# Kernel tuning notes

Hardware: AMD Instinct MI355X
Metric: run time of the kernel (lower is better)

The kernel has to match this reference:

```python
import jax, jax.numpy as jnp
import numpy as np
from jax import lax

INPUT_SIZE = 64          # classifier ROI size (init kwarg)
IMG = 640                # source image H=W
PROV, ALPHA, AD = 38, 25, 35
CONF_THRES, IOU_THRES = 0.25, 0.45
MAX_DET = 300            # yolov5 NMS max detections
FLAT = 16 * (INPUT_SIZE // 2) ** 2  # 16384


def setup_inputs() -> dict:
    key = jax.random.key(0)
    ks = jax.random.split(key, 12)
    B, N = 1, 25200
    xy = jax.random.uniform(ks[0], (B, N, 2), minval=32.0, maxval=608.0)
    wh = jax.random.uniform(ks[1], (B, N, 2), minval=16.0, maxval=128.0)
    obj = jax.random.uniform(ks[2], (B, N, 1))
    cls = jax.random.uniform(ks[3], (B, N, 1))
    preds = jnp.concatenate([xy, wh, obj, cls], axis=-1)  # [1,N,6] xywh+obj+cls
    image = jax.random.normal(ks[4], (B, 3, IMG, IMG), dtype=jnp.float32)
    W_conv = 0.1 * jax.random.normal(ks[5], (16, 3, 3, 3), dtype=jnp.float32)
    b_conv = jnp.zeros((16,), jnp.float32)
    W1 = 0.01 * jax.random.normal(ks[6], (8, FLAT, 128), dtype=jnp.float32)
    b1 = jnp.zeros((8, 128), jnp.float32)
    W2p = 0.05 * jax.random.normal(ks[7], (128, PROV), dtype=jnp.float32)
    b2p = jnp.zeros((PROV,), jnp.float32)
    W2a = 0.05 * jax.random.normal(ks[8], (128, ALPHA), dtype=jnp.float32)
    b2a = jnp.zeros((ALPHA,), jnp.float32)
    W2d = 0.05 * jax.random.normal(ks[9], (6, 128, AD), dtype=jnp.float32)
    b2d = jnp.zeros((6, AD), jnp.float32)
    return {"preds": preds, "image": image, "W_conv": W_conv, "b_conv": b_conv,
            "W1": W1, "b1": b1, "W2p": W2p, "b2p": b2p, "W2a": W2a, "b2a": b2a,
            "W2d": W2d, "b2d": b2d}


def _pairwise_iou(b):
    # b: [K,4] xyxy
    x1, y1, x2, y2 = b[:, 0], b[:, 1], b[:, 2], b[:, 3]
    area = (x2 - x1) * (y2 - y1)
    iw = jnp.clip(jnp.minimum(x2[:, None], x2[None, :]) - jnp.maximum(x1[:, None], x1[None, :]), 0.0)
    ih = jnp.clip(jnp.minimum(y2[:, None], y2[None, :]) - jnp.maximum(y1[:, None], y1[None, :]), 0.0)
    inter = iw * ih
    return inter / (area[:, None] + area[None, :] - inter + 1e-7)


def reference(preds, image, W_conv, b_conv, W1, b1, W2p, b2p, W2a, b2a, W2d, b2d):
    # ---- NMS (yolov5-style, single class) ----
    p = preds[0]                                   # [N,6]
    score = p[:, 4] * p[:, 5]                      # obj_conf * cls_conf
    xy, wh = p[:, 0:2], p[:, 2:4]
    boxes = jnp.concatenate([xy - wh / 2, xy + wh / 2], axis=-1)  # xyxy
    masked = jnp.where(score > CONF_THRES, score, -jnp.inf)
    top_s, idx = lax.top_k(masked, MAX_DET)        # sorted desc
    b = boxes[idx]                                 # [K,4]
    valid = top_s > CONF_THRES
    ious = _pairwise_iou(b)                        # [K,K]
    ar = jnp.arange(MAX_DET)

    def body(i, keep):
        sup = jnp.any((ious[i] > IOU_THRES) & keep & (ar < i))
        return keep.at[i].set(keep[i] & jnp.logical_not(sup))

    keep = lax.fori_loop(0, MAX_DET, body, valid)  # greedy suppression

    # ---- fixed-size ROI crop at box top-left (clipped) ----
    x1 = jnp.clip(jnp.round(b[:, 0]).astype(jnp.int32), 0, IMG - INPUT_SIZE)
    y1 = jnp.clip(jnp.round(b[:, 1]).astype(jnp.int32), 0, IMG - INPUT_SIZE)
    img0 = image[0]                                # [3,H,W]
    crops = jax.vmap(lambda y, x: lax.dynamic_slice(img0, (0, y, x), (3, INPUT_SIZE, INPUT_SIZE)))(y1, x1)

    # ---- LicensePlateClassifier: conv->relu->maxpool->flatten->8 heads ----
    conv = lax.conv_general_dilated(crops, W_conv, (1, 1), 'SAME',
                                    dimension_numbers=('NCHW', 'OIHW', 'NCHW'))
    conv = jax.nn.relu(conv + b_conv[None, :, None, None])
    pooled = lax.reduce_window(conv, -jnp.inf, lax.max, (1, 1, 2, 2), (1, 1, 2, 2), 'VALID')
    feats = pooled.reshape(MAX_DET, FLAT)          # NCHW flatten == torch.flatten(x,1)
    h = jax.nn.relu(jnp.einsum('kf,hfd->hkd', feats, W1) + b1[:, None, :])  # [8,K,128]
    out_p = h[0] @ W2p + b2p                       # [K,38]
    out_a = h[1] @ W2a + b2a                       # [K,25]
    out_d = jnp.einsum('hkd,hdo->hko', h[2:], W2d) + b2d[:, None, :]        # [6,K,35]
    out_d = out_d.transpose(1, 0, 2).reshape(MAX_DET, 6 * AD)
    logits = jnp.concatenate([out_p, out_a, out_d], axis=1)  # [K,273]
    return logits * keep.astype(logits.dtype)[:, None]
```

## Files before the change

kernel.cpp:

```cpp
#include <hip/hip_runtime.h>

#define N_PRED 25200
#define CONF 0.25f
#define IOU_THR 0.45f
#define MAXD 300
#define IMGW 640
#define CROPW 64
#define HISTN 16640
#define KSPLIT 16

typedef float f32x4 __attribute__((ext_vector_type(4)));
typedef short s16x8 __attribute__((ext_vector_type(8)));
typedef unsigned long long u64;

#define OFF_HIST   0u
#define OFF_CNT    66560u
#define OFF_CUT    66624u
#define OFF_CAND   66816u
#define CTRL_BYTES 75008u
#define OFF_BOXES  75008u
#define OFF_XY1    79872u
#define OFF_VALID  82432u
#define OFF_KEEP   83712u
#define OFF_SUP    84992u
#define OFF_H      97024u
#define OFF_FEATS  1325824u
#define OFF_PART   11811584u

__device__ inline unsigned short f2bf(float x) {
  unsigned u = __float_as_uint(x);
  u += 0x7FFFu + ((u >> 16) & 1u);
  return (unsigned short)(u >> 16);
}

__global__ __launch_bounds__(256) void k_hist(const float* __restrict__ preds,
                                              unsigned* __restrict__ hist) {
  int i = blockIdx.x * 256 + threadIdx.x;
  if (i >= N_PRED) return;
  float s = preds[i * 6 + 4] * preds[i * 6 + 5];
  if (s > CONF) atomicAdd(&hist[__float_as_uint(s) >> 16], 1u);
}

__global__ __launch_bounds__(256) void k_findcut(const unsigned* __restrict__ hist,
                                                 unsigned* __restrict__ cut) {
  __shared__ unsigned s[256];
  int t = threadIdx.x;
  int base = t * 65;
  unsigned local = 0;
  for (int i = 0; i < 65; ++i) local += hist[base + i];
  s[t] = local;
  __syncthreads();
  for (int off = 1; off < 256; off <<= 1) {
    unsigned add = (t + off < 256) ? s[t + off] : 0u;
    __syncthreads();
    s[t] += add;
    __syncthreads();
  }
  unsigned incl = s[t];
  unsigned excl = (t < 255) ? s[t + 1] : 0u;
  if (incl >= (unsigned)MAXD && excl < (unsigned)MAXD) {
    unsigned acc = excl, res = 0u;
    #pragma unroll
    for (int ii = 64; ii >= 0; --ii) {
      acc += hist[base + ii];
      if (res == 0u && acc >= (unsigned)MAXD) res = (unsigned)(base + ii);
    }
    cut[0] = res;
  }
}

__global__ __launch_bounds__(256) void k_compact(const float* __restrict__ preds,
                                                 const unsigned* __restrict__ cut,
                                                 unsigned* __restrict__ cnt,
                                                 u64* __restrict__ cand) {
  int i = blockIdx.x * 256 + threadIdx.x;
  if (i >= N_PRED) return;
  float s = preds[i * 6 + 4] * preds[i * 6 + 5];
  if (s <= CONF) return;
  unsigned bits = __float_as_uint(s);
  if ((bits >> 16) < cut[0]) return;
  unsigned pos = atomicAdd(cnt, 1u);
  if (pos < 1024u)
    cand[pos] = ((u64)bits << 32) | (u64)(0xFFFFFFFFu - (unsigned)i);
}

__global__ __launch_bounds__(1024) void k_sortprep(const float* __restrict__ preds,
                                                   const u64* __restrict__ cand,
                                                   float* __restrict__ boxes,
                                                   int* __restrict__ xy1,
                                                   float* __restrict__ validf) {
  __shared__ u64 sk[1024];
  int t = threadIdx.x;
  sk[t] = cand[t];
  __syncthreads();
  for (int k = 2; k <= 1024; k <<= 1)
    for (int j = k >> 1; j > 0; j >>= 1) {
      int p = t ^ j;
      if (p > t) {
        u64 a = sk[t], b = sk[p];
        bool up = ((t & k) == 0);
        bool sw = up ? (a < b) : (a > b);
        if (sw) { sk[t] = b; sk[p] = a; }
      }
      __syncthreads();
    }
  if (t < MAXD) {
    u64 key = sk[t];
    if (key != 0ull) {
      int idx = (int)(0xFFFFFFFFu - (unsigned)(key & 0xFFFFFFFFull));
      float cx = preds[idx * 6 + 0], cy = preds[idx * 6 + 1];
      float w  = preds[idx * 6 + 2], h  = preds[idx * 6 + 3];
      float x1 = cx - w * 0.5f, y1 = cy - h * 0.5f;
      float x2 = cx + w * 0.5f, y2 = cy + h * 0.5f;
      boxes[t * 4 + 0] = x1; boxes[t * 4 + 1] = y1;
      boxes[t * 4 + 2] = x2; boxes[t * 4 + 3] = y2;
      int xi = (int)rintf(x1); xi = min(max(xi, 0), IMGW - CROPW);
      int yi = (int)rintf(y1); yi = min(max(yi, 0), IMGW - CROPW);
      xy1[t * 2 + 0] = xi; xy1[t * 2 + 1] = yi;
      validf[t] = 1.0f;
    } else {
      boxes[t * 4 + 0] = 0.f; boxes[t * 4 + 1] = 0.f;
      boxes[t * 4 + 2] = 0.f; boxes[t * 4 + 3] = 0.f;
      xy1[t * 2 + 0] = 0; xy1[t * 2 + 1] = 0;
      validf[t] = 0.f;
    }
  }
}

__global__ __launch_bounds__(320) void k_iou(const float* __restrict__ boxes,
                                             u64* __restrict__ sup) {
  int i = blockIdx.x, t = threadIdx.x;
  int w = t >> 6, lane = t & 63;
  f32x4 bi = *(const f32x4*)&boxes[i * 4];
  f32x4 bj = (t < MAXD) ? *(const f32x4*)&boxes[t * 4]
                        : (f32x4){0.f, 0.f, 0.f, 0.f};
  float ar  = (bi[2] - bi[0]) * (bi[3] - bi[1]);
  float arj = (bj[2] - bj[0]) * (bj[3] - bj[1]);
  float iw = fmaxf(fminf(bi[2], bj[2]) - fmaxf(bi[0], bj[0]), 0.f);
  float ih = fmaxf(fminf(bi[3], bj[3]) - fmaxf(bi[1], bj[1]), 0.f);
  float inter = iw * ih;
  float iou = inter / (ar + arj - inter + 1e-7f);
  u64 bm = __ballot((t < MAXD) && (iou > IOU_THR));
  if (lane == 0) sup[i * 5 + w] = bm;
}

__global__ __launch_bounds__(64) void k_nms(const u64* __restrict__ sup,
                                            const float* __restrict__ validf,
                                            float* __restrict__ keepf) {
  int lane = threadIdx.x;
  u64 srow[5][5];
  #pragma unroll
  for (int c = 0; c < 5; ++c)
    #pragma unroll
    for (int ww = 0; ww < 5; ++ww) srow[c][ww] = 0ull;
  #pragma unroll
  for (int c = 0; c < 5; ++c) {
    int i = c * 64 + lane;
    if (i < MAXD) {
      #pragma unroll
      for (int ww = 0; ww <= c; ++ww) srow[c][ww] = sup[i * 5 + ww];
    }
  }
  u64 validm[5];
  #pragma unroll
  for (int c = 0; c < 5; ++c) {
    int i = c * 64 + lane;
    float vf = (i < MAXD) ? validf[i] : 0.f;
    validm[c] = __ballot(vf > 0.5f);
  }
  u64 kw0 = 0, kw1 = 0, kw2 = 0, kw3 = 0;
  #pragma unroll
  for (int c = 0; c < 5; ++c) {
    bool ext = ((srow[c][0] & kw0) | (srow[c][1] & kw1) |
                (srow[c][2] & kw2) | (srow[c][3] & kw3)) != 0ull;
    u64 alive = validm[c] & __ballot(!ext);
    unsigned mlo = (unsigned)srow[c][c], mhi = (unsigned)(srow[c][c] >> 32);
    u64 rem = alive;
    while (rem) {
      int b = (int)__builtin_ctzll(rem);
      u64 gt = (b == 63) ? 0ull : (~0ull << (b + 1));
      u64 mi = ((u64)(unsigned)__builtin_amdgcn_readlane((int)mhi, b) << 32) |
               (u64)(unsigned)__builtin_amdgcn_readlane((int)mlo, b);
      alive &= ~(mi & gt);
      rem = alive & gt;
    }
    int i = c * 64 + lane;
    if (i < MAXD) keepf[i] = ((alive >> lane) & 1ull) ? 1.f : 0.f;
    if (c == 0) kw0 = alive;
    else if (c == 1) kw1 = alive;
    else if (c == 2) kw2 = alive;
    else if (c == 3) kw3 = alive;
  }
}

__global__ __launch_bounds__(256) void k_cropconv(const float* __restrict__ image,
                                                  const float* __restrict__ Wc,
                                                  const float* __restrict__ bc,
                                                  const int* __restrict__ xy1,
                                                  short* __restrict__ feats) {
  __shared__ __align__(16) float crop[3][10][68];
  int det = blockIdx.x, sl = blockIdx.y, tid = threadIdx.x;
  int pr0 = sl * 4;
  int gyBase = pr0 * 2 - 1;
  int ch = tid >> 4, px = tid & 15;

  float w[27];
  #pragma unroll
  for (int i = 0; i < 27; i++) w[i] = Wc[ch * 27 + i];
  float bias = bc[ch];

  int x0 = xy1[det * 2 + 0], y0 = xy1[det * 2 + 1];
  float sv[8];
  #pragma unroll
  for (int i = 0; i < 8; i++) {
    int u = tid + i * 256;
    float v = 0.f;
    if (u < 1920) {
      int row = u >> 6, x = u & 63;
      int c = row / 10, ry = row - c * 10;
      int gy = gyBase + ry;
      if (gy >= 0 && gy < CROPW)
        v = image[(size_t)c * (IMGW * IMGW) + (y0 + gy) * IMGW + x0 + x];
    }
    sv[i] = v;
  }
  if (tid < 120) {
    int row = tid >> 2, e = tid & 3;
    int c = row / 10, ry = row - c * 10;
    crop[c][ry][(e == 0) ? 0 : (64 + e)] = 0.f;
  }
  #pragma unroll
  for (int i = 0; i < 8; i++) {
    int u = tid + i * 256;
    if (u < 1920) {
      int row = u >> 6, x = u & 63;
      int c = row / 10, ry = row - c * 10;
      crop[c][ry][x + 1] = sv[i];
    }
  }
  __syncthreads();
  #pragma unroll
  for (int pr = 0; pr < 4; pr++) {
    float acc0[4] = {0.f, 0.f, 0.f, 0.f};
    float acc1[4] = {0.f, 0.f, 0.f, 0.f};
    #pragma unroll
    for (int c = 0; c < 3; c++) {
      #pragma unroll
      for (int r = 0; r < 4; r++) {
        const float* rp = &crop[c][2 * pr + r][4 * px];
        f32x4 v4 = *(const f32x4*)rp;
        float2 v2 = *(const float2*)(rp + 4);
        float in[6] = {v4[0], v4[1], v4[2], v4[3], v2.x, v2.y};
        if (r <= 2) {
          const float w0 = w[c * 9 + r * 3], w1 = w[c * 9 + r * 3 + 1],
                      w2 = w[c * 9 + r * 3 + 2];
          #pragma unroll
          for (int q = 0; q < 4; q++)
            acc0[q] += in[q] * w0 + in[q + 1] * w1 + in[q + 2] * w2;
        }
        if (r >= 1) {
          const float w0 = w[c * 9 + (r - 1) * 3], w1 = w[c * 9 + (r - 1) * 3 + 1],
                      w2 = w[c * 9 + (r - 1) * 3 + 2];
          #pragma unroll
          for (int q = 0; q < 4; q++)
            acc1[q] += in[q] * w0 + in[q + 1] * w1 + in[q + 2] * w2;
        }
      }
    }
    float m0 = fmaxf(fmaxf(acc0[0], acc0[1]), fmaxf(acc1[0], acc1[1]));
    float m1 = fmaxf(fmaxf(acc0[2], acc0[3]), fmaxf(acc1[2], acc1[3]));
    unsigned lo = f2bf(fmaxf(m0 + bias, 0.f));
    unsigned hi = f2bf(fmaxf(m1 + bias, 0.f));
    *(unsigned*)&feats[(size_t)det * 16384 + ch * 1024 + (pr0 + pr) * 32 + 2 * px] =
        lo | (hi << 16);
  }
}

__global__ __launch_bounds__(512, 2) void k_gemm(const short* __restrict__ feats,
                                                 const float* __restrict__ W1,
                                                 float* __restrict__ part) {
  __shared__ __align__(16) short As[2][320 * 64];
  int tid = threadIdx.x;
  int wid = tid >> 6, lane = tid & 63;
  int wm = wid & 3, wn = wid >> 2;
  int lr = lane & 15, kg = lane >> 4;
  int ks = blockIdx.x, hd = blockIdx.y, dh = blockIdx.z;
  const int f0 = ks * 1024, d0 = dh * 64;
  const float* w1h = W1 + (size_t)hd * 16384 * 128;

  f32x4 acc[5][2];
  #pragma unroll
  for (int i = 0; i < 5; i++)
    #pragma unroll
    for (int j = 0; j < 2; j++) acc[i][j] = (f32x4){0.f, 0.f, 0.f, 0.f};

  s16x8 aR[5];
  #pragma unroll
  for (int i = 0; i < 5; i++) {
    int ch = tid + i * 512, m = ch >> 3, c = ch & 7;
    aR[i] = *(const s16x8*)(feats + (size_t)m * 16384 + f0 + c * 8);
  }
  const float* bp = w1h + (size_t)(f0 + kg * 8) * 128 + d0 + wn * 32 + lr;
  float bF[2][2][8];
  #pragma unroll
  for (int k32 = 0; k32 < 2; k32++)
    #pragma unroll
    for (int nf = 0; nf < 2; nf++)
      #pragma unroll
      for (int j = 0; j < 8; j++)
        bF[k32][nf][j] = bp[(k32 * 32 + j) * 128 + nf * 16];
  #pragma unroll
  for (int i = 0; i < 5; i++) {
    int ch = tid + i * 512, m = ch >> 3, c = ch & 7;
    *(s16x8*)((char*)&As[0][0] + m * 128 + ((c ^ (m & 7)) << 4)) = aR[i];
  }
  __syncthreads();

  for (int t = 0; t < 16; ++t) {
    int cur = t & 1;
    s16x8 bfr[2][2];
    #pragma unroll
    for (int k32 = 0; k32 < 2; k32++)
      #pragma unroll
      for (int nf = 0; nf < 2; nf++)
        #pragma unroll
        for (int j = 0; j < 8; j++)
          bfr[k32][nf][j] = (short)f2bf(bF[k32][nf][j]);
    bool pf = (t + 1) < 16;
    if (pf) {
      int f1 = f0 + (t + 1) * 64;
      #pragma unroll
      for (int i = 0; i < 5; i++) {
        int ch = tid + i * 512, m = ch >> 3, c = ch & 7;
        aR[i] = *(const s16x8*)(feats + (size_t)m * 16384 + f1 + c * 8);
      }
      const float* bp2 = bp + (size_t)(t + 1) * 64 * 128;
      #pragma unroll
      for (int k32 = 0; k32 < 2; k32++)
        #pragma unroll
        for (int nf = 0; nf < 2; nf++)
          #pragma unroll
          for (int j = 0; j < 8; j++)
            bF[k32][nf][j] = bp2[(k32 * 32 + j) * 128 + nf * 16];
    }
    #pragma unroll
    for (int k32 = 0; k32 < 2; ++k32) {
      s16x8 af[5];
      #pragma unroll
      for (int mf = 0; mf < 5; ++mf) {
        int row = wm * 80 + mf * 16 + lr;
        int c = k32 * 4 + kg;
        af[mf] = *(const s16x8*)((const char*)&As[cur][0] + row * 128 + ((c ^ (row & 7)) << 4));
      }
      #pragma unroll
      for (int nf = 0; nf < 2; ++nf)
        #pragma unroll
        for (int mf = 0; mf < 5; ++mf)
          acc[mf][nf] = __builtin_amdgcn_mfma_f32_16x16x32_bf16(af[mf], bfr[k32][nf], acc[mf][nf], 0, 0, 0);
    }
    if (pf) {
      #pragma unroll
      for (int i = 0; i < 5; i++) {
        int ch = tid + i * 512, m = ch >> 3, c = ch & 7;
        *(s16x8*)((char*)&As[cur ^ 1][0] + m * 128 + ((c ^ (m & 7)) << 4)) = aR[i];
      }
      __syncthreads();
    }
  }
  #pragma unroll
  for (int mf = 0; mf < 5; ++mf)
    #pragma unroll
    for (int nf = 0; nf < 2; ++nf)
      #pragma unroll
      for (int r = 0; r < 4; ++r) {
        int m = wm * 80 + mf * 16 + kg * 4 + r;
        int d = d0 + wn * 32 + nf * 16 + lr;
        part[(((size_t)ks * 8 + hd) * 320 + m) * 128 + d] = acc[mf][nf][r];
      }
}

__global__ __launch_bounds__(256) void k_reduce(const float* __restrict__ part,
                                                const float* __restrict__ b1,
                                                float* __restrict__ h) {
  int o4 = blockIdx.x * 256 + threadIdx.x;
  int d4 = o4 & 31;
  int k = (o4 >> 5) % 300;
  int hh = o4 / (32 * 300);
  f32x4 s = (f32x4){0.f, 0.f, 0.f, 0.f};
  #pragma unroll
  for (int ksp = 0; ksp < KSPLIT; ksp++) {
    f32x4 v = *(const f32x4*)&part[(((size_t)ksp * 8 + hh) * 320 + k) * 128 + d4 * 4];
    s[0] += v[0]; s[1] += v[1]; s[2] += v[2]; s[3] += v[3];
  }
  f32x4 b = *(const f32x4*)&b1[hh * 128 + d4 * 4];
  f32x4 r;
  #pragma unroll
  for (int j = 0; j < 4; j++) r[j] = fmaxf(s[j] + b[j], 0.f);
  *(f32x4*)&h[((size_t)hh * 300 + k) * 128 + d4 * 4] = r;
}

__global__ __launch_bounds__(320) void k_fc2(const float* __restrict__ h,
                                             const float* __restrict__ keepf,
                                             const float* __restrict__ W2p,
                                             const float* __restrict__ b2p,
                                             const float* __restrict__ W2a,
                                             const float* __restrict__ b2a,
                                             const float* __restrict__ W2d,
                                             const float* __restrict__ b2d,
                                             float* __restrict__ out) {
  int det = blockIdx.x, t = threadIdx.x;
  __shared__ float hl[1024];
  for (int i = t; i < 1024; i += 320) {
    int hh = i >> 7, d = i & 127;
    hl[i] = h[((size_t)hh * 300 + det) * 128 + d];
  }
  __syncthreads();
  if (t >= 273) return;
  float kf = keepf[det];
  float s = 0.f, bias;
  if (t < 38) {
    const float* hp = hl;
    for (int d = 0; d < 128; d++) s += hp[d] * W2p[d * 38 + t];
    bias = b2p[t];
  } else if (t < 63) {
    int c = t - 38;
    const float* hp = hl + 128;
    for (int d = 0; d < 128; d++) s += hp[d] * W2a[d * 25 + c];
    bias = b2a[c];
  } else {
    int u = t - 63, j = u / 35, o = u - j * 35;
    const float* hp = hl + (2 + j) * 128;
    for (int d = 0; d < 128; d++) s += hp[d] * W2d[((size_t)j * 128 + d) * 35 + o];
    bias = b2d[j * 35 + o];
  }
  out[det * 273 + t] = (s + bias) * kf;
}

extern "C" void kernel_launch(void* const* d_in, const int* in_sizes, int n_in,
                              void* d_out, int out_size, void* d_ws, size_t ws_size,
                              hipStream_t stream) {
  (void)in_sizes; (void)n_in; (void)out_size; (void)ws_size;
  const float* preds = (const float*)d_in[0];
  const float* image = (const float*)d_in[1];
  const float* Wc    = (const float*)d_in[2];
  const float* bc    = (const float*)d_in[3];
  const float* W1    = (const float*)d_in[4];
  const float* b1    = (const float*)d_in[5];
  const float* W2p   = (const float*)d_in[6];
  const float* b2p   = (const float*)d_in[7];
  const float* W2a   = (const float*)d_in[8];
  const float* b2a   = (const float*)d_in[9];
  const float* W2d   = (const float*)d_in[10];
  const float* b2d   = (const float*)d_in[11];

  char* ws = (char*)d_ws;
  unsigned* hist   = (unsigned*)(ws + OFF_HIST);
  unsigned* cnt    = (unsigned*)(ws + OFF_CNT);
  unsigned* cut    = (unsigned*)(ws + OFF_CUT);
  u64*      cand   = (u64*)(ws + OFF_CAND);
  float*    boxes  = (float*)(ws + OFF_BOXES);
  int*      xy1    = (int*)(ws + OFF_XY1);
  float*    validf = (float*)(ws + OFF_VALID);
  float*    keepf  = (float*)(ws + OFF_KEEP);
  u64*      sup    = (u64*)(ws + OFF_SUP);
  float*    hbuf   = (float*)(ws + OFF_H);
  short*    feats  = (short*)(ws + OFF_FEATS);
  float*    part   = (float*)(ws + OFF_PART);
  float*    out    = (float*)d_out;

  hipMemsetAsync(ws, 0, CTRL_BYTES, stream);
  k_hist<<<(N_PRED + 255) / 256, 256, 0, stream>>>(preds, hist);
  k_findcut<<<1, 256, 0, stream>>>(hist, cut);
  k_compact<<<(N_PRED + 255) / 256, 256, 0, stream>>>(preds, cut, cnt, cand);
  k_sortprep<<<1, 1024, 0, stream>>>(preds, cand, boxes, xy1, validf);
  k_iou<<<MAXD, 320, 0, stream>>>(boxes, sup);
  k_nms<<<1, 64, 0, stream>>>(sup, validf, keepf);
  k_cropconv<<<dim3(300, 8), 256, 0, stream>>>(image, Wc, bc, xy1, feats);
  k_gemm<<<dim3(KSPLIT, 8, 2), 512, 0, stream>>>(feats, W1, part);
  k_reduce<<<300, 256, 0, stream>>>(part, b1, hbuf);
  k_fc2<<<MAXD, 320, 0, stream>>>(hbuf, keepf, W2p, b2p, W2a, b2a, W2d, b2d, out);
}
```

Baseline: 123.9 us.

## Fuse NMS pipeline kernels into one cooperative kernel with grid syncs

Replaces six separate NMS-stage launches (histogram, cut search, compaction, sort, IoU, greedy NMS) with a single cooperative kernel of 32 blocks of 1024 threads that uses grid.sync between phases. The goal is to remove per-launch overhead and inter-kernel gaps on this latency-bound chain. The cost is that grid-wide barriers may be slower than kernel boundaries, fewer blocks run the IoU stage, and the cut search now scans 17 bins per thread across 1024 threads.

```diff
diff --git a/kernel.cpp b/kernel.cpp
--- a/kernel.cpp
+++ b/kernel.cpp
@@ -1,4 +1,7 @@
 #include <hip/hip_runtime.h>
+#include <hip/hip_cooperative_groups.h>
+
+namespace cg = cooperative_groups;
 
 #define N_PRED 25200
 #define CONF 0.25f
@@ -8,6 +11,7 @@
 #define CROPW 64
 #define HISTN 16640
 #define KSPLIT 16
+#define DET_BLOCKS 32
 
 typedef float f32x4 __attribute__((ext_vector_type(4)));
 typedef short s16x8 __attribute__((ext_vector_type(8)));
@@ -33,163 +37,182 @@
   return (unsigned short)(u >> 16);
 }
 
-__global__ __launch_bounds__(256) void k_hist(const float* __restrict__ preds,
-                                              unsigned* __restrict__ hist) {
-  int i = blockIdx.x * 256 + threadIdx.x;
-  if (i >= N_PRED) return;
-  float s = preds[i * 6 + 4] * preds[i * 6 + 5];
-  if (s > CONF) atomicAdd(&hist[__float_as_uint(s) >> 16], 1u);
-}
-
-__global__ __launch_bounds__(256) void k_findcut(const unsigned* __restrict__ hist,
-                                                 unsigned* __restrict__ cut) {
-  __shared__ unsigned s[256];
-  int t = threadIdx.x;
-  int base = t * 65;
-  unsigned local = 0;
-  for (int i = 0; i < 65; ++i) local += hist[base + i];
-  s[t] = local;
+__global__ __launch_bounds__(1024) void k_detect(const float* __restrict__ preds,
+                                                 unsigned* __restrict__ hist,
+                                                 unsigned* __restrict__ cut,
+                                                 unsigned* __restrict__ cnt,
+                                                 u64* __restrict__ cand,
+                                                 float* __restrict__ boxes,
+                                                 int* __restrict__ xy1,
+                                                 float* __restrict__ validf,
+                                                 u64* __restrict__ sup,
+                                                 float* __restrict__ keepf) {
+  cg::grid_group grid = cg::this_grid();
+  __shared__ unsigned su[1024];
+  __shared__ u64 sk[1024];
+  __shared__ __align__(16) float sbf[MAXD * 4];
+  int tid = threadIdx.x, bid = blockIdx.x;
+  int gt = bid * 1024 + tid;
+
+  if (gt < N_PRED) {
+    float s = preds[gt * 6 + 4] * preds[gt * 6 + 5];
+    if (s > CONF) atomicAdd(&hist[__float_as_uint(s) >> 16], 1u);
+  }
+  __threadfence();
+  grid.sync();
+
+  if (bid == 0) {
+    int base = tid * 17;
+    unsigned local = 0;
+    for (int i = 0; i < 17; ++i) {
+      int idx = base + i;
+      if (idx < HISTN) local += hist[idx];
+    }
+    su[tid] = local;
+    __syncthreads();
+    for (int off = 1; off < 1024; off <<= 1) {
+      unsigned add = (tid + off < 1024) ? su[tid + off] : 0u;
+      __syncthreads();
+      su[tid] += add;
+      __syncthreads();
+    }
+    unsigned incl = su[tid];
+    unsigned excl = (tid < 1023) ? su[tid + 1] : 0u;
+    if (incl >= (unsigned)MAXD && excl < (unsigned)MAXD) {
+      unsigned acc = excl, res = 0u;
+      for (int ii = 16; ii >= 0; --ii) {
+        int idx = base + ii;
+        if (idx < HISTN) {
+          acc += hist[idx];
+          if (res == 0u && acc >= (unsigned)MAXD) res = (unsigned)idx;
+        }
+      }
+      cut[0] = res;
+    }
+  }
+  __threadfence();
+  grid.sync();
+
+  unsigned cutv = cut[0];
+  if (gt < N_PRED) {
+    float s = preds[gt * 6 + 4] * preds[gt * 6 + 5];
+    if (s > CONF) {
+      unsigned bits = __float_as_uint(s);
+      if ((bits >> 16) >= cutv) {
+        unsigned pos = atomicAdd(cnt, 1u);
+        if (pos < 1024u)
+          cand[pos] = ((u64)bits << 32) | (u64)(0xFFFFFFFFu - (unsigned)gt);
+      }
+    }
+  }
+  __threadfence();
+  grid.sync();
+
+  if (bid == 0) {
+    sk[tid] = cand[tid];
+    __syncthreads();
+    for (int k = 2; k <= 1024; k <<= 1)
+      for (int j = k >> 1; j > 0; j >>= 1) {
+        int p = tid ^ j;
+        if (p > tid) {
+          u64 a = sk[tid], b = sk[p];
+          bool up = ((tid & k) == 0);
+          bool sw = up ? (a < b) : (a > b);
+          if (sw) { sk[tid] = b; sk[p] = a; }
+        }
+        __syncthreads();
+      }
+    if (tid < MAXD) {
+      u64 key = sk[tid];
+      if (key != 0ull) {
+        int idx = (int)(0xFFFFFFFFu - (unsigned)(key & 0xFFFFFFFFull));
+        float cx = preds[idx * 6 + 0], cy = preds[idx * 6 + 1];
+        float w  = preds[idx * 6 + 2], h  = preds[idx * 6 + 3];
+        float x1 = cx - w * 0.5f, y1 = cy - h * 0.5f;
+        float x2 = cx + w * 0.5f, y2 = cy + h * 0.5f;
+        boxes[tid * 4 + 0] = x1; boxes[tid * 4 + 1] = y1;
+        boxes[tid * 4 + 2] = x2; boxes[tid * 4 + 3] = y2;
+        int xi = (int)rintf(x1); xi = min(max(xi, 0), IMGW - CROPW);
+        int yi = (int)rintf(y1); yi = min(max(yi, 0), IMGW - CROPW);
+        xy1[tid * 2 + 0] = xi; xy1[tid * 2 + 1] = yi;
+        validf[tid] = 1.0f;
+      } else {
+        boxes[tid * 4 + 0] = 0.f; boxes[tid * 4 + 1] = 0.f;
+        boxes[tid * 4 + 2] = 0.f; boxes[tid * 4 + 3] = 0.f;
+        xy1[tid * 2 + 0] = 0; xy1[tid * 2 + 1] = 0;
+        validf[tid] = 0.f;
+      }
+    }
+  }
+  __threadfence();
+  grid.sync();
+
+  for (int i = tid; i < MAXD * 4; i += 1024) sbf[i] = boxes[i];
   __syncthreads();
-  for (int off = 1; off < 256; off <<= 1) {
-    unsigned add = (t + off < 256) ? s[t + off] : 0u;
-    __syncthreads();
-    s[t] += add;
-    __syncthreads();
-  }
-  unsigned incl = s[t];
-  unsigned excl = (t < 255) ? s[t + 1] : 0u;
-  if (incl >= (unsigned)MAXD && excl < (unsigned)MAXD) {
-    unsigned acc = excl, res = 0u;
-    #pragma unroll
-    for (int ii = 64; ii >= 0; --ii) {
-      acc += hist[base + ii];
-      if (res == 0u && acc >= (unsigned)MAXD) res = (unsigned)(base + ii);
-    }
-    cut[0] = res;
-  }
-}
-
-__global__ __launch_bounds__(256) void k_compact(const float* __restrict__ preds,
-                                                 const unsigned* __restrict__ cut,
-                                                 unsigned* __restrict__ cnt,
-                                                 u64* __restrict__ cand) {
-  int i = blockIdx.x * 256 + threadIdx.x;
-  if (i >= N_PRED) return;
-  float s = preds[i * 6 + 4] * preds[i * 6 + 5];
-  if (s <= CONF) return;
-  unsigned bits = __float_as_uint(s);
-  if ((bits >> 16) < cut[0]) return;
-  unsigned pos = atomicAdd(cnt, 1u);
-  if (pos < 1024u)
-    cand[pos] = ((u64)bits << 32) | (u64)(0xFFFFFFFFu - (unsigned)i);
-}
-
-__global__ __launch_bounds__(1024) void k_sortprep(const float* __restrict__ preds,
-                                                   const u64* __restrict__ cand,
-                                                   float* __restrict__ boxes,
-                                                   int* __restrict__ xy1,
-                                                   float* __restrict__ validf) {
-  __shared__ u64 sk[1024];
-  int t = threadIdx.x;
-  sk[t] = cand[t];
-  __syncthreads();
-  for (int k = 2; k <= 1024; k <<= 1)
-    for (int j = k >> 1; j > 0; j >>= 1) {
-      int p = t ^ j;
-      if (p > t) {
-        u64 a = sk[t], b = sk[p];
-        bool up = ((t & k) == 0);
-        bool sw = up ? (a < b) : (a > b);
-        if (sw) { sk[t] = b; sk[p] = a; }
-      }
-      __syncthreads();
-    }
-  if (t < MAXD) {
-    u64 key = sk[t];
-    if (key != 0ull) {
-      int idx = (int)(0xFFFFFFFFu - (unsigned)(key & 0xFFFFFFFFull));
-      float cx = preds[idx * 6 + 0], cy = preds[idx * 6 + 1];
-      float w  = preds[idx * 6 + 2], h  = preds[idx * 6 + 3];
-      float x1 = cx - w * 0.5f, y1 = cy - h * 0.5f;
-      float x2 = cx + w * 0.5f, y2 = cy + h * 0.5f;
-      boxes[t * 4 + 0] = x1; boxes[t * 4 + 1] = y1;
-      boxes[t * 4 + 2] = x2; boxes[t * 4 + 3] = y2;
-      int xi = (int)rintf(x1); xi = min(max(xi, 0), IMGW - CROPW);
-      int yi = (int)rintf(y1); yi = min(max(yi, 0), IMGW - CROPW);
-      xy1[t * 2 + 0] = xi; xy1[t * 2 + 1] = yi;
-      validf[t] = 1.0f;
-    } else {
-      boxes[t * 4 + 0] = 0.f; boxes[t * 4 + 1] = 0.f;
-      boxes[t * 4 + 2] = 0.f; boxes[t * 4 + 3] = 0.f;
-      xy1[t * 2 + 0] = 0; xy1[t * 2 + 1] = 0;
-      validf[t] = 0.f;
-    }
-  }
-}
-
-__global__ __launch_bounds__(320) void k_iou(const float* __restrict__ boxes,
-                                             u64* __restrict__ sup) {
-  int i = blockIdx.x, t = threadIdx.x;
-  int w = t >> 6, lane = t & 63;
-  f32x4 bi = *(const f32x4*)&boxes[i * 4];
-  f32x4 bj = (t < MAXD) ? *(const f32x4*)&boxes[t * 4]
-                        : (f32x4){0.f, 0.f, 0.f, 0.f};
-  float ar  = (bi[2] - bi[0]) * (bi[3] - bi[1]);
-  float arj = (bj[2] - bj[0]) * (bj[3] - bj[1]);
-  float iw = fmaxf(fminf(bi[2], bj[2]) - fmaxf(bi[0], bj[0]), 0.f);
-  float ih = fmaxf(fminf(bi[3], bj[3]) - fmaxf(bi[1], bj[1]), 0.f);
-  float inter = iw * ih;
-  float iou = inter / (ar + arj - inter + 1e-7f);
-  u64 bm = __ballot((t < MAXD) && (iou > IOU_THR));
-  if (lane == 0) sup[i * 5 + w] = bm;
-}
-
-__global__ __launch_bounds__(64) void k_nms(const u64* __restrict__ sup,
-                                            const float* __restrict__ validf,
-                                            float* __restrict__ keepf) {
-  int lane = threadIdx.x;
-  u64 srow[5][5];
-  #pragma unroll
-  for (int c = 0; c < 5; ++c)
-    #pragma unroll
-    for (int ww = 0; ww < 5; ++ww) srow[c][ww] = 0ull;
-  #pragma unroll
-  for (int c = 0; c < 5; ++c) {
-    int i = c * 64 + lane;
-    if (i < MAXD) {
-      #pragma unroll
-      for (int ww = 0; ww <= c; ++ww) srow[c][ww] = sup[i * 5 + ww];
-    }
-  }
-  u64 validm[5];
-  #pragma unroll
-  for (int c = 0; c < 5; ++c) {
-    int i = c * 64 + lane;
-    float vf = (i < MAXD) ? validf[i] : 0.f;
-    validm[c] = __ballot(vf > 0.5f);
-  }
-  u64 kw0 = 0, kw1 = 0, kw2 = 0, kw3 = 0;
-  #pragma unroll
-  for (int c = 0; c < 5; ++c) {
-    bool ext = ((srow[c][0] & kw0) | (srow[c][1] & kw1) |
-                (srow[c][2] & kw2) | (srow[c][3] & kw3)) != 0ull;
-    u64 alive = validm[c] & __ballot(!ext);
-    unsigned mlo = (unsigned)srow[c][c], mhi = (unsigned)(srow[c][c] >> 32);
-    u64 rem = alive;
-    while (rem) {
-      int b = (int)__builtin_ctzll(rem);
-      u64 gt = (b == 63) ? 0ull : (~0ull << (b + 1));
-      u64 mi = ((u64)(unsigned)__builtin_amdgcn_readlane((int)mhi, b) << 32) |
-               (u64)(unsigned)__builtin_amdgcn_readlane((int)mlo, b);
-      alive &= ~(mi & gt);
-      rem = alive & gt;
-    }
-    int i = c * 64 + lane;
-    if (i < MAXD) keepf[i] = ((alive >> lane) & 1ull) ? 1.f : 0.f;
-    if (c == 0) kw0 = alive;
-    else if (c == 1) kw1 = alive;
-    else if (c == 2) kw2 = alive;
-    else if (c == 3) kw3 = alive;
+  if (tid < 320) {
+    int w = tid >> 6, lane = tid & 63;
+    f32x4 bj = (tid < MAXD) ? *(const f32x4*)&sbf[tid * 4]
+                            : (f32x4){0.f, 0.f, 0.f, 0.f};
+    float arj = (bj[2] - bj[0]) * (bj[3] - bj[1]);
+    for (int row = bid; row < MAXD; row += DET_BLOCKS) {
+      f32x4 bi = *(const f32x4*)&sbf[row * 4];
+      float ar = (bi[2] - bi[0]) * (bi[3] - bi[1]);
+      float iw = fmaxf(fminf(bi[2], bj[2]) - fmaxf(bi[0], bj[0]), 0.f);
+      float ih = fmaxf(fminf(bi[3], bj[3]) - fmaxf(bi[1], bj[1]), 0.f);
+      float inter = iw * ih;
+      float iou = inter / (ar + arj - inter + 1e-7f);
+      u64 bm = __ballot((tid < MAXD) && (iou > IOU_THR));
+      if (lane == 0) sup[row * 5 + w] = bm;
+    }
+  }
+  __threadfence();
+  grid.sync();
+
+  if (bid == 0 && tid < 64) {
+    int lane = tid;
+    u64 srow[5][5];
+    #pragma unroll
+    for (int c = 0; c < 5; ++c)
+      #pragma unroll
+      for (int ww = 0; ww < 5; ++ww) srow[c][ww] = 0ull;
+    #pragma unroll
+    for (int c = 0; c < 5; ++c) {
+      int i = c * 64 + lane;
+      if (i < MAXD) {
+        #pragma unroll
+        for (int ww = 0; ww <= c; ++ww) srow[c][ww] = sup[i * 5 + ww];
+      }
+    }
+    u64 validm[5];
+    #pragma unroll
+    for (int c = 0; c < 5; ++c) {
+      int i = c * 64 + lane;
+      float vf = (i < MAXD) ? validf[i] : 0.f;
+      validm[c] = __ballot(vf > 0.5f);
+    }
+    u64 kw0 = 0, kw1 = 0, kw2 = 0, kw3 = 0;
+    #pragma unroll
+    for (int c = 0; c < 5; ++c) {
+      bool ext = ((srow[c][0] & kw0) | (srow[c][1] & kw1) |
+                  (srow[c][2] & kw2) | (srow[c][3] & kw3)) != 0ull;
+      u64 alive = validm[c] & __ballot(!ext);
+      unsigned mlo = (unsigned)srow[c][c], mhi = (unsigned)(srow[c][c] >> 32);
+      u64 rem = alive;
+      while (rem) {
+        int b = (int)__builtin_ctzll(rem);
+        u64 gtm = (b == 63) ? 0ull : (~0ull << (b + 1));
+        u64 mi = ((u64)(unsigned)__builtin_amdgcn_readlane((int)mhi, b) << 32) |
+                 (u64)(unsigned)__builtin_amdgcn_readlane((int)mlo, b);
+        alive &= ~(mi & gtm);
+        rem = alive & gtm;
+      }
+      int i = c * 64 + lane;
+      if (i < MAXD) keepf[i] = ((alive >> lane) & 1ull) ? 1.f : 0.f;
+      if (c == 0) kw0 = alive;
+      else if (c == 1) kw1 = alive;
+      else if (c == 2) kw2 = alive;
+      else if (c == 3) kw3 = alive;
+    }
   }
 }
 
@@ -469,12 +492,11 @@
   float*    out    = (float*)d_out;
 
   hipMemsetAsync(ws, 0, CTRL_BYTES, stream);
-  k_hist<<<(N_PRED + 255) / 256, 256, 0, stream>>>(preds, hist);
-  k_findcut<<<1, 256, 0, stream>>>(hist, cut);
-  k_compact<<<(N_PRED + 255) / 256, 256, 0, stream>>>(preds, cut, cnt, cand);
-  k_sortprep<<<1, 1024, 0, stream>>>(preds, cand, boxes, xy1, validf);
-  k_iou<<<MAXD, 320, 0, stream>>>(boxes, sup);
-  k_nms<<<1, 64, 0, stream>>>(sup, validf, keepf);
+  void* dargs[] = {(void*)&preds, (void*)&hist, (void*)&cut, (void*)&cnt,
+                   (void*)&cand, (void*)&boxes, (void*)&xy1, (void*)&validf,
+                   (void*)&sup, (void*)&keepf};
+  hipLaunchCooperativeKernel((const void*)k_detect, dim3(DET_BLOCKS), dim3(1024),
+                             dargs, 0, stream);
   k_cropconv<<<dim3(300, 8), 256, 0, stream>>>(image, Wc, bc, xy1, feats);
   k_gemm<<<dim3(KSPLIT, 8, 2), 512, 0, stream>>>(feats, W1, part);
   k_reduce<<<300, 256, 0, stream>>>(part, b1, hbuf);
```

Result: slower. 192.4 us (+55.2%).
